# Performance work log

Hardware: AMD Instinct MI355X
Metric: run time of the kernel (lower is better)

## Reference

```python
import jax, jax.numpy as jnp
import numpy as np

B, N, D, H = 64, 197, 768, 12
HD = D // H          # 64
MLP = 4 * D          # 3072
WIN = 14
NUM_REL = (2 * WIN - 1) * (2 * WIN - 1) + 3  # 732
SCALE = HD ** -0.5
DCF_SCALE = 1.0
EPS = 1e-5


def _make_rel_index(wh, ww):
    coords = np.stack(np.meshgrid(np.arange(wh), np.arange(ww), indexing='ij'))  # [2, wh, ww]
    flat = coords.reshape(2, -1)
    rel = flat[:, :, None] - flat[:, None, :]          # [2, L, L]
    rel = rel.transpose(1, 2, 0).astype(np.int64)      # [L, L, 2]
    rel[..., 0] += wh - 1
    rel[..., 1] += ww - 1
    rel[..., 0] *= 2 * ww - 1
    idx = np.zeros((wh * ww + 1, wh * ww + 1), dtype=np.int32)
    idx[1:, 1:] = rel.sum(-1)
    nrd = (2 * wh - 1) * (2 * ww - 1) + 3
    idx[0, :] = nrd - 3
    idx[:, 0] = nrd - 2
    idx[0, 0] = nrd - 1
    return idx


def _ln(x, w, b):
    m = x.mean(-1, keepdims=True)
    v = ((x - m) ** 2).mean(-1, keepdims=True)
    return (x - m) * jax.lax.rsqrt(v + EPS) * w + b


def setup_inputs() -> dict:
    key = jax.random.key(0)
    ks = jax.random.split(key, 32)
    rnd = lambda i, shp, s=0.02: jax.random.normal(ks[i], shp, jnp.float32) * s
    return {
        'x': jax.random.normal(ks[0], (B, N, D), jnp.float32),
        'w_qkv': rnd(1, (3 * D, D)),
        'q_bias': rnd(2, (D,)),
        'v_bias': rnd(3, (D,)),
        'ssf_scale_qkv': 1.0 + rnd(4, (3 * D,)),
        'ssf_shift_qkv': rnd(5, (3 * D,)),
        'rel_bias_table': rnd(6, (NUM_REL, H)),
        'bases_coeff': rnd(7, (H, H)),
        'w_proj': rnd(8, (D, D)),
        'b_proj': rnd(9, (D,)),
        'ssf_scale_proj': 1.0 + rnd(10, (D,)),
        'ssf_shift_proj': rnd(11, (D,)),
        'norm1_w': jnp.ones((D,), jnp.float32),
        'norm1_b': jnp.zeros((D,), jnp.float32),
        'norm2_w': jnp.ones((D,), jnp.float32),
        'norm2_b': jnp.zeros((D,), jnp.float32),
        'ssf_scale_1': 1.0 + rnd(12, (D,)),
        'ssf_shift_1': rnd(13, (D,)),
        'ssf_scale_2': 1.0 + rnd(14, (D,)),
        'ssf_shift_2': rnd(15, (D,)),
        'w_fc1': rnd(16, (MLP, D)),
        'b_fc1': rnd(17, (MLP,)),
        'w_fc2': rnd(18, (D, MLP)),
        'b_fc2': rnd(19, (D,)),
        'ssf_scale_mlp': 1.0 + rnd(20, (D,)),
        'ssf_shift_mlp': rnd(21, (D,)),
        'gamma_1': jnp.full((D,), 0.1, jnp.float32),
        'gamma_2': jnp.full((D,), 0.1, jnp.float32),
        'rel_pos_index': jnp.asarray(_make_rel_index(WIN, WIN)),
    }


def reference(x, w_qkv, q_bias, v_bias, ssf_scale_qkv, ssf_shift_qkv,
              rel_bias_table, bases_coeff, w_proj, b_proj,
              ssf_scale_proj, ssf_shift_proj, norm1_w, norm1_b, norm2_w, norm2_b,
              ssf_scale_1, ssf_shift_1, ssf_scale_2, ssf_shift_2,
              w_fc1, b_fc1, w_fc2, b_fc2, ssf_scale_mlp, ssf_shift_mlp,
              gamma_1, gamma_2, rel_pos_index):
    # --- attention branch (eval mode: all dropouts are identity) ---
    h = _ln(x, norm1_w, norm1_b) * ssf_scale_1 + ssf_shift_1
    qkv_bias = jnp.concatenate([q_bias, jnp.zeros_like(v_bias), v_bias])
    qkv = h @ w_qkv.T + qkv_bias                       # [B, N, 3D]
    qkv = qkv * ssf_scale_qkv + ssf_shift_qkv
    qkv = qkv.reshape(B, N, 3, H, HD).transpose(2, 0, 3, 1, 4)  # [3, B, H, N, hd]
    q, k, v = qkv[0] * SCALE, qkv[1], qkv[2]
    attn = jnp.einsum('bhnd,bhmd->bhnm', q, k)         # [B, H, N, N]
    bias = rel_bias_table[rel_pos_index.reshape(-1)].reshape(N, N, H).transpose(2, 0, 1)
    attn = jax.nn.softmax(attn + bias[None], axis=-1)
    # dcf head mixing
    coeff = bases_coeff.T * DCF_SCALE + jnp.eye(H, dtype=attn.dtype)
    attn = jnp.einsum('bhnl,hk->bknl', attn, coeff)
    y = jnp.einsum('bhnm,bhmd->bnhd', attn, v).reshape(B, N, D)
    y = y @ w_proj.T + b_proj
    y = y * ssf_scale_proj + ssf_shift_proj
    x = x + gamma_1 * y
    # --- MLP branch ---
    h = _ln(x, norm2_w, norm2_b) * ssf_scale_2 + ssf_shift_2
    m = jax.nn.gelu(h @ w_fc1.T + b_fc1, approximate=False)
    m = m @ w_fc2.T + b_fc2
    m = m * ssf_scale_mlp + ssf_shift_mlp
    return x + gamma_2 * m
```

## Files before the change

kernel.cpp:

```cpp
#include <hip/hip_runtime.h>

typedef unsigned short u16;
using f32x4  = __attribute__((ext_vector_type(4))) float;
using bf16x8 = __attribute__((ext_vector_type(8))) __bf16;

#define Bz   64
#define Nn   197
#define Dd   768
#define Hh   12
#define HDp  64
#define MLPD 3072
#define ROWS (Bz*Nn)
#define NM   (Nn*Nn)
#define NPAD 224

#define OFF_H    0UL
#define OFF_X1   19365888UL
#define OFF_BIA  58097664UL
#define OFF_WB   59960496UL
#define OFF_CH   74116272UL
#define WQKV_E 0UL
#define WPRJ_E 1769472UL
#define WFC1_E 2359296UL
#define WFC2_E 4718592UL
#define QKV_B  907776UL
#define P_B    1059072UL
#define VT_B   344064UL
#define CHUNK_B 2310912UL

__device__ inline float b2f(u16 v){ unsigned u = ((unsigned)v) << 16; float f; __builtin_memcpy(&f,&u,4); return f; }
__device__ inline u16 f2b(float f){ unsigned u; __builtin_memcpy(&u,&f,4); u += 0x7FFFu + ((u>>16)&1u); return (u16)(u>>16); }

__device__ inline float gelu_f(float x){
    float z  = fabsf(x) * 0.70710678118f;
    float t  = 1.f / (1.f + 0.3275911f * z);
    float y  = t*(0.254829592f + t*(-0.284496736f + t*(1.421413741f + t*(-1.453152027f + t*1.061405429f))));
    float er = 1.f - y * __expf(-z*z);
    er = copysignf(er, x);
    return 0.5f * x * (1.f + er);
}

__device__ inline void gload_lds16(const u16* g, u16* l) {
    __builtin_amdgcn_global_load_lds((const __attribute__((address_space(1))) void*)g,
                                     (__attribute__((address_space(3))) void*)l, 16, 0, 0);
}

__global__ __launch_bounds__(256)
void conv_b16(const float* __restrict__ src, u16* __restrict__ dst, int n4)
{
    int t = blockIdx.x*256 + threadIdx.x;
    if (t >= n4) return;
    float4 v = *(const float4*)(src + (size_t)t*4);
    u16* d = dst + (size_t)t*4;
    d[0] = f2b(v.x); d[1] = f2b(v.y); d[2] = f2b(v.z); d[3] = f2b(v.w);
}

template<int EPI, int BN, int TH>
__global__ __launch_bounds__(TH)
void gemmv(const u16* __restrict__ A, const u16* __restrict__ W, void* __restrict__ Cp,
           int M, int N, int K, int lda, int ldw,
           const float* __restrict__ e0, const float* __restrict__ e1,
           const float* __restrict__ e2, const float* __restrict__ e3,
           const float* __restrict__ ef)
{
    extern __shared__ u16 lds[];
    constexpr int BM   = 256;
    constexpr int SWEEP = TH * 8;
    constexpr int ICA  = (BM * 32) / SWEEP;
    constexpr int ICB  = (BN * 32) / SWEEP;
    constexpr int VN   = ICA + ICB;
    constexpr int ASZ  = BM * 32;
    constexpr int BSZ  = BN * 32;
    constexpr int ABUF = 2 * ASZ;
    constexpr int BBUF = 2 * BSZ;
    constexpr int WCN  = BN / 64;
    constexpr int MF   = 4;
    constexpr int MH   = 2;

    u16* sA = lds;
    u16* sB = lds + 2 * ABUF;

    const int tid  = threadIdx.x;
    const int lane = tid & 63;
    const int wave = tid >> 6;
    const int wr   = wave / WCN;
    const int wc   = wave % WCN;
    const int rid  = lane & 15;
    const int kg   = lane >> 4;
    const int m0   = blockIdx.y * BM;
    const int n0   = blockIdx.x * BN;
    const int t8   = tid * 8;

    const u16* asrc[2][ICA]; int adst[2][ICA];
    const u16* bsrc[2][ICB]; int bdst[2][ICB];
#pragma unroll
    for (int s = 0; s < 2; ++s) {
#pragma unroll
        for (int i = 0; i < ICA; ++i) {
            int e = i*SWEEP + t8, r = e >> 5;
            int g = ((e >> 3) & 3) ^ ((r >> 1) & 3);
            int row = m0 + r; if (row > M-1) row = M-1;
            asrc[s][i] = A + (size_t)row*lda + s*32 + g*8;
            adst[s][i] = s*ASZ + e;
        }
#pragma unroll
        for (int i = 0; i < ICB; ++i) {
            int e = i*SWEEP + t8, r = e >> 5;
            int g = ((e >> 3) & 3) ^ ((r >> 1) & 3);
            int col = n0 + r; if (col > N-1) col = N-1;
            bsrc[s][i] = W + (size_t)col*ldw + s*32 + g*8;
            bdst[s][i] = s*BSZ + e;
        }
    }

    const int koA   = (kg ^ ((rid >> 1) & 3)) * 8;
    const int aRow0 = (wr*64 + rid) * 32 + koA;
    const int bRow  = (wc*64 + rid) * 32 + koA;

    f32x4 acc[MF][4];
#pragma unroll
    for (int i = 0; i < MF; ++i)
#pragma unroll
        for (int j = 0; j < 4; ++j) acc[i][j] = (f32x4){0.f,0.f,0.f,0.f};

#define WAITBAR() do { \
        if constexpr (VN == 2)      asm volatile("s_waitcnt vmcnt(2) lgkmcnt(0)\n\ts_barrier" ::: "memory"); \
        else if constexpr (VN == 3) asm volatile("s_waitcnt vmcnt(3) lgkmcnt(0)\n\ts_barrier" ::: "memory"); \
        else                        asm volatile("s_waitcnt vmcnt(4) lgkmcnt(0)\n\ts_barrier" ::: "memory"); \
    } while (0)

#pragma unroll
    for (int i = 0; i < ICA; ++i) gload_lds16(asrc[0][i], sA + adst[0][i]);
#pragma unroll
    for (int i = 0; i < ICB; ++i) gload_lds16(bsrc[0][i], sB + bdst[0][i]);
    asm volatile("" ::: "memory");
#pragma unroll
    for (int i = 0; i < ICA; ++i) gload_lds16(asrc[1][i], sA + adst[1][i]);
#pragma unroll
    for (int i = 0; i < ICB; ++i) gload_lds16(bsrc[1][i], sB + bdst[1][i]);
    WAITBAR();

    const int NT = K >> 6;
    for (int t = 0; t < NT; ++t) {
        const int p  = t & 1;
        const size_t kpre = (size_t)(t + 1) * 64;
        const u16* paB = sA + p * ABUF;
        const u16* pbB = sB + p * BBUF;
        const int  qa  = (p ^ 1) * ABUF;
        const int  qb  = (p ^ 1) * BBUF;
        bf16x8 af[MH], wf[4];

        {
            const u16* pa = paB + aRow0;
#pragma unroll
            for (int f = 0; f < MH; ++f) af[f] = *(const bf16x8*)(pa + f*512);
            const u16* pb = pbB + bRow;
#pragma unroll
            for (int j = 0; j < 4; ++j) wf[j] = *(const bf16x8*)(pb + j*512);
#pragma unroll
            for (int i = 0; i < ICA; ++i) gload_lds16(asrc[0][i] + kpre, sA + adst[0][i] + qa);
            __builtin_amdgcn_s_setprio(1);
#pragma unroll
            for (int f = 0; f < MH; ++f)
#pragma unroll
                for (int j = 0; j < 4; ++j)
                    acc[f][j] = __builtin_amdgcn_mfma_f32_16x16x32_bf16(af[f], wf[j], acc[f][j], 0, 0, 0);
            __builtin_amdgcn_s_setprio(0);
        }
        {
            const u16* pa = paB + aRow0 + MH*512;
#pragma unroll
            for (int f = 0; f < MH; ++f) af[f] = *(const bf16x8*)(pa + f*512);
#pragma unroll
            for (int i = 0; i < ICB; ++i) gload_lds16(bsrc[0][i] + kpre, sB + bdst[0][i] + qb);
            __builtin_amdgcn_s_setprio(1);
#pragma unroll
            for (int f = 0; f < MH; ++f)
#pragma unroll
                for (int j = 0; j < 4; ++j)
                    acc[MH+f][j] = __builtin_amdgcn_mfma_f32_16x16x32_bf16(af[f], wf[j], acc[MH+f][j], 0, 0, 0);
            __builtin_amdgcn_s_setprio(0);
        }
        WAITBAR();
        {
            const u16* pa = paB + ASZ + aRow0;
#pragma unroll
            for (int f = 0; f < MH; ++f) af[f] = *(const bf16x8*)(pa + f*512);
            const u16* pb = pbB + BSZ + bRow;
#pragma unroll
            for (int j = 0; j < 4; ++j) wf[j] = *(const bf16x8*)(pb + j*512);
#pragma unroll
            for (int i = 0; i < ICA; ++i) gload_lds16(asrc[1][i] + kpre, sA + adst[1][i] + qa);
            __builtin_amdgcn_s_setprio(1);
#pragma unroll
            for (int f = 0; f < MH; ++f)
#pragma unroll
                for (int j = 0; j < 4; ++j)
                    acc[f][j] = __builtin_amdgcn_mfma_f32_16x16x32_bf16(af[f], wf[j], acc[f][j], 0, 0, 0);
            __builtin_amdgcn_s_setprio(0);
        }
        {
            const u16* pa = paB + ASZ + aRow0 + MH*512;
#pragma unroll
            for (int f = 0; f < MH; ++f) af[f] = *(const bf16x8*)(pa + f*512);
#pragma unroll
            for (int i = 0; i < ICB; ++i) gload_lds16(bsrc[1][i] + kpre, sB + bdst[1][i] + qb);
            __builtin_amdgcn_s_setprio(1);
#pragma unroll
            for (int f = 0; f < MH; ++f)
#pragma unroll
                for (int j = 0; j < 4; ++j)
                    acc[MH+f][j] = __builtin_amdgcn_mfma_f32_16x16x32_bf16(af[f], wf[j], acc[MH+f][j], 0, 0, 0);
            __builtin_amdgcn_s_setprio(0);
        }
        WAITBAR();
    }
    asm volatile("s_waitcnt vmcnt(0)" ::: "memory");
    __syncthreads();
#undef WAITBAR

    float* ka = (float*)lds;
    float* kb = ka + BN;
    if (tid < BN) {
        int gn = n0 + tid;
        if constexpr (EPI == 0) {
            float mql = (gn < 768) ? 0.125f : 1.f;
            float bias = 0.f;
            if (gn < 768) bias = e0[gn];
            else if (gn >= 1536) bias = e1[gn-1536];
            float sc = e2[gn];
            ka[tid] = sc * mql;
            kb[tid] = (bias * sc + e3[gn]) * mql;
        } else if constexpr (EPI == 4) {
            ka[tid] = 0.f;
            kb[tid] = e0[gn];
        } else {
            float sc = e1[gn];
            ka[tid] = sc;
            kb[tid] = e0[gn]*sc + e2[gn];
        }
    }
    __syncthreads();
    const int rq = (lane >> 4) * 4;
    const int cc = lane & 15;
    float kaj[4], kbj[4];
#pragma unroll
    for (int j = 0; j < 4; ++j) {
        int c = wc*64 + j*16 + cc;
        kaj[j] = ka[c]; kbj[j] = kb[c];
    }
    __syncthreads();

    if constexpr (EPI == 0 || EPI == 4) {
        u16* ct = lds;
#pragma unroll
        for (int i = 0; i < MF; ++i) {
#pragma unroll
            for (int j = 0; j < 4; ++j) {
#pragma unroll
                for (int r = 0; r < 4; ++r) {
                    int rowL = wr*64 + i*16 + rq + r;
                    int col  = wc*64 + j*16 + cc;
                    float v = acc[i][j][r];
                    u16 o;
                    if constexpr (EPI == 0) o = f2b(v*kaj[j] + kbj[j]);
                    else                    o = f2b(gelu_f(v + kbj[j]));
                    ct[rowL*264 + col] = o;
                }
            }
        }
        __syncthreads();
        constexpr int ldc = (EPI == 0) ? 2304 : 3072;
        u16* C = (u16*)Cp;
        constexpr int RPS = TH / 32;
#pragma unroll
        for (int sw = 0; sw < 256/RPS; ++sw) {
            int rowL = sw*RPS + (tid >> 5);
            int gm = m0 + rowL;
            if (gm < M) {
                int col0 = (tid & 31) * 8;
                *(uint4*)(C + (size_t)gm*ldc + n0 + col0) =
                    *(const uint4*)(ct + rowL*264 + col0);
            }
        }
    } else {
        float* cf = (float*)lds;
        float* C = (float*)Cp;
#pragma unroll
        for (int h = 0; h < 2; ++h) {
            if ((wr >> 1) == h) {
#pragma unroll
                for (int i = 0; i < MF; ++i) {
#pragma unroll
                    for (int j = 0; j < 4; ++j) {
#pragma unroll
                        for (int r = 0; r < 4; ++r) {
                            int rowH = (wr & 1)*64 + i*16 + rq + r;
                            int col  = wc*64 + j*16 + cc;
                            cf[rowH*132 + col] = acc[i][j][r]*kaj[j] + kbj[j];
                        }
                    }
                }
            }
            __syncthreads();
#pragma unroll
            for (int sw = 0; sw < 8; ++sw) {
                int rowH = sw*16 + (tid >> 5);
                int gm = m0 + h*128 + rowH;
                if (gm < M) {
                    int col0 = (tid & 31) * 4;
                    f32x4 v  = *(const f32x4*)(cf + rowH*132 + col0);
                    size_t gidx = (size_t)gm*768 + n0 + col0;
                    f32x4 xv = *(const f32x4*)(ef + gidx);
                    f32x4 g3 = *(const f32x4*)(e3 + n0 + col0);
                    f32x4 o;
#pragma unroll
                    for (int q = 0; q < 4; ++q) o[q] = xv[q] + g3[q]*v[q];
                    *(f32x4*)(C + gidx) = o;
                }
            }
            __syncthreads();
        }
    }
}

template<int EPI>
__global__ __launch_bounds__(256, 2)
void gemm128p(const u16* __restrict__ A, const u16* __restrict__ W, void* __restrict__ Cp,
              int M, int N, int K, int lda, int ldw,
              const float* __restrict__ e0, const float* __restrict__ e1,
              const float* __restrict__ e2, const float* __restrict__ e3,
              const float* __restrict__ e4, const float* __restrict__ ef)
{
    extern __shared__ u16 lds[];
    constexpr int SWEEP = 2048;
    constexpr int ICA  = 2;
    constexpr int ICB  = 2;
    constexpr int ASZ  = 128 * 32;
    constexpr int BSZ  = 128 * 32;
    constexpr int ABUF = 2 * ASZ;
    constexpr int BBUF = 2 * BSZ;
    constexpr int MF   = 4;
    constexpr int MH   = 2;

    u16* sA = lds;
    u16* sB = lds + 2 * ABUF;

    const int tid  = threadIdx.x;
    const int lane = tid & 63;
    const int wave = tid >> 6;
    const int wr   = wave >> 1;
    const int wc   = wave & 1;
    const int rid  = lane & 15;
    const int kg   = lane >> 4;
    const int m0   = blockIdx.y * 128;
    const int n0   = blockIdx.x * 128;
    const int t8   = tid * 8;

    const u16* asrc[2][ICA]; int adst[2][ICA];
    const u16* bsrc[2][ICB]; int bdst[2][ICB];
#pragma unroll
    for (int s = 0; s < 2; ++s) {
#pragma unroll
        for (int i = 0; i < ICA; ++i) {
            int e = i*SWEEP + t8, r = e >> 5;
            int g = ((e >> 3) & 3) ^ ((r >> 1) & 3);
            int row = m0 + r; if (row > M-1) row = M-1;
            asrc[s][i] = A + (size_t)row*lda + s*32 + g*8;
            adst[s][i] = s*ASZ + e;
        }
#pragma unroll
        for (int i = 0; i < ICB; ++i) {
            int e = i*SWEEP + t8, r = e >> 5;
            int g = ((e >> 3) & 3) ^ ((r >> 1) & 3);
            int col = n0 + r; if (col > N-1) col = N-1;
            bsrc[s][i] = W + (size_t)col*ldw + s*32 + g*8;
            bdst[s][i] = s*BSZ + e;
        }
    }

    const int koA   = (kg ^ ((rid >> 1) & 3)) * 8;
    const int aRow0 = (wr*64 + rid) * 32 + koA;
    const int bRow  = (wc*64 + rid) * 32 + koA;

    f32x4 acc[MF][4];
#pragma unroll
    for (int i = 0; i < MF; ++i)
#pragma unroll
        for (int j = 0; j < 4; ++j) acc[i][j] = (f32x4){0.f,0.f,0.f,0.f};

#define WAITBAR() asm volatile("s_waitcnt vmcnt(4) lgkmcnt(0)\n\ts_barrier" ::: "memory")

#pragma unroll
    for (int i = 0; i < ICA; ++i) gload_lds16(asrc[0][i], sA + adst[0][i]);
#pragma unroll
    for (int i = 0; i < ICB; ++i) gload_lds16(bsrc[0][i], sB + bdst[0][i]);
    asm volatile("" ::: "memory");
#pragma unroll
    for (int i = 0; i < ICA; ++i) gload_lds16(asrc[1][i], sA + adst[1][i]);
#pragma unroll
    for (int i = 0; i < ICB; ++i) gload_lds16(bsrc[1][i], sB + bdst[1][i]);
    WAITBAR();

    const int NT = K >> 6;
    for (int t = 0; t < NT; ++t) {
        const int p  = t & 1;
        const size_t kpre = (size_t)(t + 1) * 64;
        const u16* paB = sA + p * ABUF;
        const u16* pbB = sB + p * BBUF;
        const int  qa  = (p ^ 1) * ABUF;
        const int  qb  = (p ^ 1) * BBUF;
        bf16x8 af[MH], wf[4];

        {
            const u16* pa = paB + aRow0;
#pragma unroll
            for (int f = 0; f < MH; ++f) af[f] = *(const bf16x8*)(pa + f*512);
            const u16* pb = pbB + bRow;
#pragma unroll
            for (int j = 0; j < 4; ++j) wf[j] = *(const bf16x8*)(pb + j*512);
#pragma unroll
            for (int i = 0; i < ICA; ++i) gload_lds16(asrc[0][i] + kpre, sA + adst[0][i] + qa);
            __builtin_amdgcn_s_setprio(1);
#pragma unroll
            for (int f = 0; f < MH; ++f)
#pragma unroll
                for (int j = 0; j < 4; ++j)
                    acc[f][j] = __builtin_amdgcn_mfma_f32_16x16x32_bf16(af[f], wf[j], acc[f][j], 0, 0, 0);
            __builtin_amdgcn_s_setprio(0);
        }
        {
            const u16* pa = paB + aRow0 + MH*512;
#pragma unroll
            for (int f = 0; f < MH; ++f) af[f] = *(const bf16x8*)(pa + f*512);
#pragma unroll
            for (int i = 0; i < ICB; ++i) gload_lds16(bsrc[0][i] + kpre, sB + bdst[0][i] + qb);
            __builtin_amdgcn_s_setprio(1);
#pragma unroll
            for (int f = 0; f < MH; ++f)
#pragma unroll
                for (int j = 0; j < 4; ++j)
                    acc[MH+f][j] = __builtin_amdgcn_mfma_f32_16x16x32_bf16(af[f], wf[j], acc[MH+f][j], 0, 0, 0);
            __builtin_amdgcn_s_setprio(0);
        }
        WAITBAR();
        {
            const u16* pa = paB + ASZ + aRow0;
#pragma unroll
            for (int f = 0; f < MH; ++f) af[f] = *(const bf16x8*)(pa + f*512);
            const u16* pb = pbB + BSZ + bRow;
#pragma unroll
            for (int j = 0; j < 4; ++j) wf[j] = *(const bf16x8*)(pb + j*512);
#pragma unroll
            for (int i = 0; i < ICA; ++i) gload_lds16(asrc[1][i] + kpre, sA + adst[1][i] + qa);
            __builtin_amdgcn_s_setprio(1);
#pragma unroll
            for (int f = 0; f < MH; ++f)
#pragma unroll
                for (int j = 0; j < 4; ++j)
                    acc[f][j] = __builtin_amdgcn_mfma_f32_16x16x32_bf16(af[f], wf[j], acc[f][j], 0, 0, 0);
            __builtin_amdgcn_s_setprio(0);
        }
        {
            const u16* pa = paB + ASZ + aRow0 + MH*512;
#pragma unroll
            for (int f = 0; f < MH; ++f) af[f] = *(const bf16x8*)(pa + f*512);
#pragma unroll
            for (int i = 0; i < ICB; ++i) gload_lds16(bsrc[1][i] + kpre, sB + bdst[1][i] + qb);
            __builtin_amdgcn_s_setprio(1);
#pragma unroll
            for (int f = 0; f < MH; ++f)
#pragma unroll
                for (int j = 0; j < 4; ++j)
                    acc[MH+f][j] = __builtin_amdgcn_mfma_f32_16x16x32_bf16(af[f], wf[j], acc[MH+f][j], 0, 0, 0);
            __builtin_amdgcn_s_setprio(0);
        }
        WAITBAR();
    }
    asm volatile("s_waitcnt vmcnt(0)" ::: "memory");
    __syncthreads();
#undef WAITBAR

    float* ka = (float*)lds;
    float* kb = ka + 128;
    if (tid < 128) {
        int gn = n0 + tid;
        float sc = e1[gn];
        ka[tid] = sc;
        kb[tid] = e0[gn]*sc + e2[gn];
    }
    __syncthreads();
    const int rq = (lane >> 4) * 4;
    const int cc = lane & 15;
    float kaj[4], kbj[4];
#pragma unroll
    for (int j = 0; j < 4; ++j) {
        int c = wc*64 + j*16 + cc;
        kaj[j] = ka[c]; kbj[j] = kb[c];
    }
    __syncthreads();

    float* cf = (float*)lds;
    const float* RES = e4;
    float* C = (float*)Cp;
#pragma unroll
    for (int h = 0; h < 2; ++h) {
        if (wr == h) {
#pragma unroll
            for (int i = 0; i < MF; ++i) {
#pragma unroll
                for (int j = 0; j < 4; ++j) {
#pragma unroll
                    for (int r = 0; r < 4; ++r) {
                        int rowH = i*16 + rq + r;
                        int col  = wc*64 + j*16 + cc;
                        cf[rowH*132 + col] = acc[i][j][r]*kaj[j] + kbj[j];
                    }
                }
            }
        }
        __syncthreads();
#pragma unroll
        for (int sw = 0; sw < 8; ++sw) {
            int rowH = sw*8 + (tid >> 5);
            int gm = m0 + h*64 + rowH;
            if (gm < M) {
                int col0 = (tid & 31) * 4;
                f32x4 v  = *(const f32x4*)(cf + rowH*132 + col0);
                size_t gidx = (size_t)gm*768 + n0 + col0;
                f32x4 xv = *(const f32x4*)(RES + gidx);
                f32x4 g3 = *(const f32x4*)(e3 + n0 + col0);
                f32x4 o;
#pragma unroll
                for (int q = 0; q < 4; ++q) o[q] = xv[q] + g3[q]*v[q];
                *(f32x4*)(C + gidx) = o;
            }
        }
        __syncthreads();
    }
}

template<int EPI>
__global__ __launch_bounds__(256)
void gemm_nt(const u16* __restrict__ A, const u16* __restrict__ W, void* __restrict__ Cp,
             int M, int N, int K, int lda, int ldw, int b0,
             const float* __restrict__ ef)
{
    __shared__ __align__(16) u16 csm[(EPI == 1) ? 32768 : 16384];
    const int tid  = threadIdx.x;
    const int lane = tid & 63;
    const int wave = tid >> 6;
    const int z    = blockIdx.z;
    const int m0   = wave*64;
    const int n0   = blockIdx.x*64;
    const int rid  = lane & 15;
    const int kq   = (lane >> 4) * 8;

    const u16* Ab = A;
    const u16* Wb = W;
    if constexpr (EPI == 1) {
        int bb = z/12, hh = z - bb*12;
        Ab = A + ((size_t)bb*Nn)*2304 + hh*64;
        Wb = W + ((size_t)bb*Nn)*2304 + 768 + hh*64;
    } else {
        Ab = A + (size_t)z*Nn*NPAD;
        Wb = W + (size_t)z*HDp*NPAD;
    }

    f32x4 acc[4][4];
#pragma unroll
    for (int i = 0; i < 4; ++i)
#pragma unroll
        for (int j = 0; j < 4; ++j) acc[i][j] = (f32x4){0.f,0.f,0.f,0.f};

    for (int k0 = 0; k0 < K; k0 += 32) {
        bf16x8 af[4], wf[4];
#pragma unroll
        for (int i = 0; i < 4; ++i) {
            int r = m0 + i*16 + rid; if (r > M-1) r = M-1;
            af[i] = *(const bf16x8*)(Ab + (size_t)r*lda + k0 + kq);
        }
#pragma unroll
        for (int j = 0; j < 4; ++j) {
            int c = n0 + j*16 + rid; if (c > N-1) c = N-1;
            wf[j] = *(const bf16x8*)(Wb + (size_t)c*ldw + k0 + kq);
        }
#pragma unroll
        for (int i = 0; i < 4; ++i)
#pragma unroll
            for (int j = 0; j < 4; ++j)
                acc[i][j] = __builtin_amdgcn_mfma_f32_16x16x32_bf16(af[i], wf[j], acc[i][j], 0, 0, 0);
    }

    const int rq = (lane >> 4) * 4;
    const int cc = lane & 15;

    if constexpr (EPI == 1) {
        float* cs = (float*)csm;
#pragma unroll
        for (int i = 0; i < 4; ++i)
#pragma unroll
            for (int j = 0; j < 4; ++j)
#pragma unroll
                for (int r = 0; r < 4; ++r)
                    cs[(m0 + i*16 + rq + r)*64 + j*16 + cc] = acc[i][j][r];
        __syncthreads();
        int hh = z - (z/12)*12;
        const float* bsrc = ef + (size_t)hh*NM;
        u16* P = (u16*)Cp + (size_t)z*Nn*NPAD;
        for (int sw = 0; sw < 13; ++sw) {
            int row = sw*16 + (tid >> 4);
            int col0 = (tid & 15) * 4;
            int gn = n0 + col0;
            if (row < Nn && gn < NPAD) {
                f32x4 v = *(const f32x4*)(cs + row*64 + col0);
                const float* bp = bsrc + (size_t)row*Nn + gn;
                float b0v = bp[0], b1v = bp[1], b2v = bp[2], b3v = bp[3];
                unsigned lo = (unsigned)f2b(v[0]+b0v) | ((unsigned)f2b(v[1]+b1v) << 16);
                unsigned hi = (unsigned)f2b(v[2]+b2v) | ((unsigned)f2b(v[3]+b3v) << 16);
                uint2 pk; pk.x = lo; pk.y = hi;
                *(uint2*)(P + (size_t)row*NPAD + gn) = pk;
            }
        }
    } else {
        u16* cs = csm;
#pragma unroll
        for (int i = 0; i < 4; ++i)
#pragma unroll
            for (int j = 0; j < 4; ++j)
#pragma unroll
                for (int r = 0; r < 4; ++r)
                    cs[(m0 + i*16 + rq + r)*64 + j*16 + cc] = f2b(acc[i][j][r]);
        __syncthreads();
        int bb = z/12, kk = z - bb*12;
        u16* Y = (u16*)Cp + ((size_t)(b0+bb)*Nn)*768 + kk*64;
        for (int sw = 0; sw < 7; ++sw) {
            int row = sw*32 + (tid >> 3);
            if (row < Nn) {
                int col0 = (tid & 7) * 8;
                *(uint4*)(Y + (size_t)row*768 + col0) = *(const uint4*)(cs + row*64 + col0);
            }
        }
    }
}

__global__ __launch_bounds__(256)
void ln_ssf(const float* __restrict__ x, const float* __restrict__ w, const float* __restrict__ bb,
            const float* __restrict__ sc, const float* __restrict__ sh, u16* __restrict__ out)
{
    const int row = blockIdx.x, tid = threadIdx.x;
    const float* xr = x + (size_t)row * 768;
    float v[3], s1 = 0.f, s2 = 0.f;
#pragma unroll
    for (int i = 0; i < 3; ++i) {
        float f = xr[tid + i*256];
        v[i] = f; s1 += f; s2 += f*f;
    }
    for (int o = 32; o > 0; o >>= 1) { s1 += __shfl_xor(s1, o); s2 += __shfl_xor(s2, o); }
    __shared__ float r1[4], r2[4];
    int wv = tid >> 6;
    if ((tid & 63) == 0) { r1[wv] = s1; r2[wv] = s2; }
    __syncthreads();
    s1 = r1[0]+r1[1]+r1[2]+r1[3];
    s2 = r2[0]+r2[1]+r2[2]+r2[3];
    float mean = s1 * (1.f/768.f);
    float var  = s2 * (1.f/768.f) - mean*mean;
    float rstd = rsqrtf(fmaxf(var, 0.f) + 1e-5f);
#pragma unroll
    for (int i = 0; i < 3; ++i) {
        int c = tid + i*256;
        float h = (v[i] - mean) * rstd * w[c] + bb[c];
        h = h * sc[c] + sh[c];
        out[(size_t)row*768 + c] = f2b(h);
    }
}

__global__ __launch_bounds__(256)
void bias_gather(const int* __restrict__ idx, const float* __restrict__ table, float* __restrict__ biasf)
{
    int t = blockIdx.x*256 + threadIdx.x;
    if (t >= NM) return;
    int id = idx[t];
#pragma unroll
    for (int h = 0; h < 12; ++h)
        biasf[(size_t)h*NM + t] = table[id*12 + h];
}

__global__ __launch_bounds__(256)
void softmax_dcf(u16* __restrict__ P, const float* __restrict__ bases, int nb)
{
    __shared__ float cf[144];
    int tid = threadIdx.x;
    if (tid < 144) {
        int k = tid / 12, h = tid - k*12;
        cf[h*12 + k] = bases[k*12 + h] + (h == k ? 1.f : 0.f);
    }
    __syncthreads();
    int ridx = blockIdx.x*4 + (tid >> 6);
    if (ridx >= nb*Nn) return;
    int lane = tid & 63;
    int m0 = lane * 4;
    int bb = ridx / Nn, n = ridx - bb*Nn;
    const size_t hs = (size_t)Nn*NPAD;
    u16* base = P + ((size_t)bb*12)*hs + (size_t)n*NPAD;

    float e[12][4];
#pragma unroll
    for (int h = 0; h < 12; ++h) {
        float s[4];
        if (m0 < NPAD) {
            uint2 pv = *(const uint2*)(base + h*hs + m0);
            s[0] = b2f((u16)(pv.x & 0xFFFF)); s[1] = b2f((u16)(pv.x >> 16));
            s[2] = b2f((u16)(pv.y & 0xFFFF)); s[3] = b2f((u16)(pv.y >> 16));
        } else { s[0]=s[1]=s[2]=s[3] = -1e30f; }
#pragma unroll
        for (int j = 0; j < 4; ++j) if (m0 + j >= Nn) s[j] = -1e30f;
        float mx = fmaxf(fmaxf(s[0], s[1]), fmaxf(s[2], s[3]));
        for (int o = 32; o > 0; o >>= 1) mx = fmaxf(mx, __shfl_xor(mx, o));
        float sum = 0.f;
#pragma unroll
        for (int j = 0; j < 4; ++j) {
            float ev = __expf(fmaxf(s[j] - mx, -80.f));
            if (m0 + j >= Nn) ev = 0.f;
            e[h][j] = ev; sum += ev;
        }
        for (int o = 32; o > 0; o >>= 1) sum += __shfl_xor(sum, o);
        float inv = 1.f / sum;
#pragma unroll
        for (int j = 0; j < 4; ++j) e[h][j] *= inv;
    }
    if (m0 < NPAD) {
#pragma unroll
        for (int k = 0; k < 12; ++k) {
            float o0 = 0.f, o1 = 0.f, o2 = 0.f, o3 = 0.f;
#pragma unroll
            for (int h = 0; h < 12; ++h) {
                float c = cf[h*12 + k];
                o0 += e[h][0]*c; o1 += e[h][1]*c; o2 += e[h][2]*c; o3 += e[h][3]*c;
            }
            unsigned lo = (unsigned)f2b(o0) | ((unsigned)f2b(o1) << 16);
            unsigned hi = (unsigned)f2b(o2) | ((unsigned)f2b(o3) << 16);
            uint2 pk; pk.x = lo; pk.y = hi;
            *(uint2*)(base + k*hs + m0) = pk;
        }
    }
}

__global__ __launch_bounds__(256)
void v_transpose(const u16* __restrict__ qkv, u16* __restrict__ vT)
{
    __shared__ u16 lds[64*198];
    int z = blockIdx.x;
    int bb = z/12, hh = z - bb*12;
    int tid = threadIdx.x;
    const u16* src = qkv + ((size_t)bb*Nn)*2304 + 1536 + hh*64;
    for (int e = tid; e < Nn*64; e += 256) {
        int m = e >> 6, d = e & 63;
        lds[d*198 + m] = src[(size_t)m*2304 + d];
    }
    __syncthreads();
    u16* dst = vT + (size_t)z*64*NPAD;
    for (int e = tid; e < 64*NPAD; e += 256) {
        int d = e / NPAD, m = e - d*NPAD;
        dst[e] = (m < Nn) ? lds[d*198 + m] : (u16)0;
    }
}

extern "C" void kernel_launch(void* const* d_in, const int* in_sizes, int n_in,
                              void* d_out, int out_size, void* d_ws, size_t ws_size,
                              hipStream_t stream)
{
    const float* x       = (const float*)d_in[0];
    const float* w_qkv   = (const float*)d_in[1];
    const float* q_bias  = (const float*)d_in[2];
    const float* v_bias  = (const float*)d_in[3];
    const float* s_qkv   = (const float*)d_in[4];
    const float* sh_qkv  = (const float*)d_in[5];
    const float* rel_tab = (const float*)d_in[6];
    const float* bases   = (const float*)d_in[7];
    const float* w_proj  = (const float*)d_in[8];
    const float* b_proj  = (const float*)d_in[9];
    const float* s_proj  = (const float*)d_in[10];
    const float* sh_proj = (const float*)d_in[11];
    const float* n1w     = (const float*)d_in[12];
    const float* n1b     = (const float*)d_in[13];
    const float* n2w     = (const float*)d_in[14];
    const float* n2b     = (const float*)d_in[15];
    const float* ss1     = (const float*)d_in[16];
    const float* ssh1    = (const float*)d_in[17];
    const float* ss2     = (const float*)d_in[18];
    const float* ssh2    = (const float*)d_in[19];
    const float* w_fc1   = (const float*)d_in[20];
    const float* b_fc1   = (const float*)d_in[21];
    const float* w_fc2   = (const float*)d_in[22];
    const float* b_fc2   = (const float*)d_in[23];
    const float* s_mlp   = (const float*)d_in[24];
    const float* sh_mlp  = (const float*)d_in[25];
    const float* g1      = (const float*)d_in[26];
    const float* g2      = (const float*)d_in[27];
    const int*   relidx  = (const int*)d_in[28];

    char*  ws   = (char*)d_ws;
    u16*   hbuf = (u16*)(ws + OFF_H);
    float* x1   = (float*)(ws + OFF_X1);
    float* bia  = (float*)(ws + OFF_BIA);
    u16*   wb   = (u16*)(ws + OFF_WB);
    float* out  = (float*)d_out;

    u16* wqkvB = wb + WQKV_E;
    u16* wprjB = wb + WPRJ_E;
    u16* wfc1B = wb + WFC1_E;
    u16* wfc2B = wb + WFC2_E;

    hipFuncSetAttribute(reinterpret_cast<const void*>(&gemmv<0,256,1024>),
                        hipFuncAttributeMaxDynamicSharedMemorySize, 139264);
    hipFuncSetAttribute(reinterpret_cast<const void*>(&gemmv<4,256,1024>),
                        hipFuncAttributeMaxDynamicSharedMemorySize, 139264);
    hipFuncSetAttribute(reinterpret_cast<const void*>(&gemmv<5,128,512>),
                        hipFuncAttributeMaxDynamicSharedMemorySize, 98304);
    hipFuncSetAttribute(reinterpret_cast<const void*>(&gemm128p<3>),
                        hipFuncAttributeMaxDynamicSharedMemorySize, 65536);

    int nb = 64;
    while (nb > 1 && OFF_CH + (size_t)nb*CHUNK_B > ws_size) nb >>= 1;
    const int nchunk = 64 / nb;
    u16* qkvC = (u16*)(ws + OFF_CH);
    u16* PC   = (u16*)(ws + OFF_CH + (size_t)nb*QKV_B);
    u16* vTC  = (u16*)(ws + OFF_CH + (size_t)nb*(QKV_B + P_B));

    conv_b16<<<dim3(1728), dim3(256), 0, stream>>>(w_qkv, wqkvB, 442368);
    conv_b16<<<dim3(576),  dim3(256), 0, stream>>>(w_proj, wprjB, 147456);
    conv_b16<<<dim3(2304), dim3(256), 0, stream>>>(w_fc1, wfc1B, 589824);
    conv_b16<<<dim3(2304), dim3(256), 0, stream>>>(w_fc2, wfc2B, 589824);

    ln_ssf<<<dim3(ROWS), dim3(256), 0, stream>>>(x, n1w, n1b, ss1, ssh1, hbuf);
    bias_gather<<<dim3(152), dim3(256), 0, stream>>>(relidx, rel_tab, bia);

    for (int c = 0; c < nchunk; ++c) {
        const int b0 = c * nb;
        const int nrows = nb * Nn;
        const int gy = (nrows + 255) / 256;
        gemmv<0,256,1024><<<dim3(9, gy), dim3(1024), 139264, stream>>>(
            hbuf + (size_t)b0*Nn*768, wqkvB, qkvC,
            nrows, 2304, 768, 768, 768, q_bias, v_bias, s_qkv, sh_qkv, nullptr);
        v_transpose<<<dim3(nb*12), dim3(256), 0, stream>>>(qkvC, vTC);
        gemm_nt<1><<<dim3(4, 1, nb*12), dim3(256), 0, stream>>>(
            qkvC, qkvC, PC, Nn, Nn, 64, 2304, 2304, 0, bia);
        softmax_dcf<<<dim3((nb*Nn + 3)/4), dim3(256), 0, stream>>>(PC, bases, nb);
        gemm_nt<2><<<dim3(1, 1, nb*12), dim3(256), 0, stream>>>(
            PC, vTC, hbuf, Nn, 64, NPAD, NPAD, NPAD, b0, nullptr);
    }

    gemm128p<3><<<dim3(6, 99), dim3(256), 65536, stream>>>(
        hbuf, wprjB, x1, ROWS, 768, 768, 768, 768,
        b_proj, s_proj, sh_proj, g1, x, nullptr);
    ln_ssf<<<dim3(ROWS), dim3(256), 0, stream>>>(x1, n2w, n2b, ss2, ssh2, hbuf);

    u16* mlpC = qkvC;
    size_t avail = (ws_size > OFF_CH) ? (ws_size - OFF_CH) : (size_t)CHUNK_B;
    int nrM = (int)(avail / (MLPD * 2));
    if (nrM < 1) nrM = 1;
    if (nrM > ROWS) nrM = ROWS;
    for (int r0 = 0; r0 < ROWS; r0 += nrM) {
        int cr = ROWS - r0; if (cr > nrM) cr = nrM;
        int gy = (cr + 255) / 256;
        gemmv<4,256,1024><<<dim3(12, gy), dim3(1024), 139264, stream>>>(
            hbuf + (size_t)r0*768, wfc1B, mlpC, cr, 3072, 768, 768, 768,
            b_fc1, nullptr, nullptr, nullptr, nullptr);
        gemmv<5,128,512><<<dim3(6, gy), dim3(512), 98304, stream>>>(
            mlpC, wfc2B, out + (size_t)r0*768, cr, 768, 3072, 3072, 3072,
            b_fc2, s_mlp, sh_mlp, g2, x1 + (size_t)r0*768);
    }
}
```

Before: 715.9 us.

## Fuse V transpose into PV GEMM and widen FC2 GEMM tile

Removes the separate v_transpose kernel. The PV GEMM now loads V straight from the qkv buffer into swizzled shared memory and reads its B fragments from there, which saves a global round trip and one launch per chunk. The FC2 GEMM switches from the 128-wide, 512-thread variant to the 256-wide, 1024-thread one, with its epilogue reworked for 64-row slices of a 260-stride LDS buffer. In exchange, each PV block repeats the strided V load, FC2 runs fewer blocks (3 columns), and the larger LDS footprint may reduce occupancy.

```diff
diff --git a/kernel.cpp b/kernel.cpp
--- a/kernel.cpp
+++ b/kernel.cpp
@@ -287,36 +287,38 @@
         float* cf = (float*)lds;
         float* C = (float*)Cp;
 #pragma unroll
-        for (int h = 0; h < 2; ++h) {
-            if ((wr >> 1) == h) {
+        for (int h = 0; h < 4; ++h) {
+            if (wr == h) {
 #pragma unroll
                 for (int i = 0; i < MF; ++i) {
 #pragma unroll
                     for (int j = 0; j < 4; ++j) {
 #pragma unroll
                         for (int r = 0; r < 4; ++r) {
-                            int rowH = (wr & 1)*64 + i*16 + rq + r;
+                            int rowH = i*16 + rq + r;
                             int col  = wc*64 + j*16 + cc;
-                            cf[rowH*132 + col] = acc[i][j][r]*kaj[j] + kbj[j];
+                            cf[rowH*260 + col] = acc[i][j][r]*kaj[j] + kbj[j];
                         }
                     }
                 }
             }
             __syncthreads();
-#pragma unroll
-            for (int sw = 0; sw < 8; ++sw) {
-                int rowH = sw*16 + (tid >> 5);
-                int gm = m0 + h*128 + rowH;
+            {
+                int row = tid >> 4;
+                int gm = m0 + h*64 + row;
                 if (gm < M) {
-                    int col0 = (tid & 31) * 4;
-                    f32x4 v  = *(const f32x4*)(cf + rowH*132 + col0);
-                    size_t gidx = (size_t)gm*768 + n0 + col0;
-                    f32x4 xv = *(const f32x4*)(ef + gidx);
-                    f32x4 g3 = *(const f32x4*)(e3 + n0 + col0);
-                    f32x4 o;
-#pragma unroll
-                    for (int q = 0; q < 4; ++q) o[q] = xv[q] + g3[q]*v[q];
-                    *(f32x4*)(C + gidx) = o;
+#pragma unroll
+                    for (int k = 0; k < 4; ++k) {
+                        int col0 = (tid & 15)*4 + k*64;
+                        f32x4 v = *(const f32x4*)(cf + row*260 + col0);
+                        size_t gidx = (size_t)gm*768 + n0 + col0;
+                        f32x4 xv = *(const f32x4*)(ef + gidx);
+                        f32x4 g3 = *(const f32x4*)(e3 + n0 + col0);
+                        f32x4 o;
+#pragma unroll
+                        for (int q = 0; q < 4; ++q) o[q] = xv[q] + g3[q]*v[q];
+                        *(f32x4*)(C + gidx) = o;
+                    }
                 }
             }
             __syncthreads();
@@ -547,6 +549,7 @@
              const float* __restrict__ ef)
 {
     __shared__ __align__(16) u16 csm[(EPI == 1) ? 32768 : 16384];
+    __shared__ __align__(16) u16 vsm[(EPI == 2) ? 64*256 : 1];
     const int tid  = threadIdx.x;
     const int lane = tid & 63;
     const int wave = tid >> 6;
@@ -563,8 +566,18 @@
         Ab = A + ((size_t)bb*Nn)*2304 + hh*64;
         Wb = W + ((size_t)bb*Nn)*2304 + 768 + hh*64;
     } else {
+        int bb = z/12, hh = z - bb*12;
         Ab = A + (size_t)z*Nn*NPAD;
-        Wb = W + (size_t)z*HDp*NPAD;
+        const u16* vsrc = W + ((size_t)bb*Nn)*2304 + 1536 + hh*64;
+        for (int e = tid; e < Nn*64; e += 256) {
+            int m = e >> 6, d = e & 63;
+            vsm[d*256 + ((((m >> 3) ^ d) & 31) << 3) + (m & 7)] = vsrc[(size_t)m*2304 + d];
+        }
+        for (int e = tid; e < 64*32; e += 256) {
+            int d = e & 63; int m = Nn + (e >> 6);
+            if (m < NPAD) vsm[d*256 + ((((m >> 3) ^ d) & 31) << 3) + (m & 7)] = 0;
+        }
+        __syncthreads();
     }
 
     f32x4 acc[4][4];
@@ -582,8 +595,14 @@
         }
 #pragma unroll
         for (int j = 0; j < 4; ++j) {
-            int c = n0 + j*16 + rid; if (c > N-1) c = N-1;
-            wf[j] = *(const bf16x8*)(Wb + (size_t)c*ldw + k0 + kq);
+            if constexpr (EPI == 1) {
+                int c = n0 + j*16 + rid; if (c > N-1) c = N-1;
+                wf[j] = *(const bf16x8*)(Wb + (size_t)c*ldw + k0 + kq);
+            } else {
+                int c = j*16 + rid;
+                int kb = (k0 + kq) >> 3;
+                wf[j] = *(const bf16x8*)(vsm + c*256 + (((kb ^ c) & 31) << 3));
+            }
         }
 #pragma unroll
         for (int i = 0; i < 4; ++i)
@@ -743,26 +762,6 @@
             uint2 pk; pk.x = lo; pk.y = hi;
             *(uint2*)(base + k*hs + m0) = pk;
         }
-    }
-}
-
-__global__ __launch_bounds__(256)
-void v_transpose(const u16* __restrict__ qkv, u16* __restrict__ vT)
-{
-    __shared__ u16 lds[64*198];
-    int z = blockIdx.x;
-    int bb = z/12, hh = z - bb*12;
-    int tid = threadIdx.x;
-    const u16* src = qkv + ((size_t)bb*Nn)*2304 + 1536 + hh*64;
-    for (int e = tid; e < Nn*64; e += 256) {
-        int m = e >> 6, d = e & 63;
-        lds[d*198 + m] = src[(size_t)m*2304 + d];
-    }
-    __syncthreads();
-    u16* dst = vT + (size_t)z*64*NPAD;
-    for (int e = tid; e < 64*NPAD; e += 256) {
-        int d = e / NPAD, m = e - d*NPAD;
-        dst[e] = (m < Nn) ? lds[d*198 + m] : (u16)0;
     }
 }
 
@@ -816,8 +815,8 @@
                         hipFuncAttributeMaxDynamicSharedMemorySize, 139264);
     hipFuncSetAttribute(reinterpret_cast<const void*>(&gemmv<4,256,1024>),
                         hipFuncAttributeMaxDynamicSharedMemorySize, 139264);
-    hipFuncSetAttribute(reinterpret_cast<const void*>(&gemmv<5,128,512>),
-                        hipFuncAttributeMaxDynamicSharedMemorySize, 98304);
+    hipFuncSetAttribute(reinterpret_cast<const void*>(&gemmv<5,256,1024>),
+                        hipFuncAttributeMaxDynamicSharedMemorySize, 139264);
     hipFuncSetAttribute(reinterpret_cast<const void*>(&gemm128p<3>),
                         hipFuncAttributeMaxDynamicSharedMemorySize, 65536);
 
@@ -826,7 +825,6 @@
     const int nchunk = 64 / nb;
     u16* qkvC = (u16*)(ws + OFF_CH);
     u16* PC   = (u16*)(ws + OFF_CH + (size_t)nb*QKV_B);
-    u16* vTC  = (u16*)(ws + OFF_CH + (size_t)nb*(QKV_B + P_B));
 
     conv_b16<<<dim3(1728), dim3(256), 0, stream>>>(w_qkv, wqkvB, 442368);
     conv_b16<<<dim3(576),  dim3(256), 0, stream>>>(w_proj, wprjB, 147456);
@@ -843,12 +841,11 @@
         gemmv<0,256,1024><<<dim3(9, gy), dim3(1024), 139264, stream>>>(
             hbuf + (size_t)b0*Nn*768, wqkvB, qkvC,
             nrows, 2304, 768, 768, 768, q_bias, v_bias, s_qkv, sh_qkv, nullptr);
-        v_transpose<<<dim3(nb*12), dim3(256), 0, stream>>>(qkvC, vTC);
         gemm_nt<1><<<dim3(4, 1, nb*12), dim3(256), 0, stream>>>(
             qkvC, qkvC, PC, Nn, Nn, 64, 2304, 2304, 0, bia);
         softmax_dcf<<<dim3((nb*Nn + 3)/4), dim3(256), 0, stream>>>(PC, bases, nb);
         gemm_nt<2><<<dim3(1, 1, nb*12), dim3(256), 0, stream>>>(
-            PC, vTC, hbuf, Nn, 64, NPAD, NPAD, NPAD, b0, nullptr);
+            PC, qkvC, hbuf, Nn, 64, NPAD, NPAD, 2304, b0, nullptr);
     }
 
     gemm128p<3><<<dim3(6, 99), dim3(256), 65536, stream>>>(
@@ -867,7 +864,7 @@
         gemmv<4,256,1024><<<dim3(12, gy), dim3(1024), 139264, stream>>>(
             hbuf + (size_t)r0*768, wfc1B, mlpC, cr, 3072, 768, 768, 768,
             b_fc1, nullptr, nullptr, nullptr, nullptr);
-        gemmv<5,128,512><<<dim3(6, gy), dim3(512), 98304, stream>>>(
+        gemmv<5,256,1024><<<dim3(3, gy), dim3(1024), 139264, stream>>>(
             mlpC, wfc2B, out + (size_t)r0*768, cr, 768, 3072, 3072, 3072,
             b_fc2, s_mlp, sh_mlp, g2, x1 + (size_t)r0*768);
     }
```

Result: faster. 659.5 us (-7.9%).
